# Kernel tuning notes

Hardware: AMD Instinct MI355X
Metric: run time of the kernel (lower is better)

## Reference

```python
import jax, jax.numpy as jnp
import numpy as np

B, A, IN, H, NA = 256, 32, 512, 512, 64


def setup_inputs() -> dict:
    key = jax.random.key(0)
    ks = jax.random.split(key, 9)
    s = 1.0 / np.sqrt(H).astype(np.float32)
    si = 1.0 / np.sqrt(IN).astype(np.float32)
    return {
        "inputs": jax.random.normal(ks[0], (B * A, IN), jnp.float32),
        "hidden_state": jnp.zeros((B, A, H), jnp.float32),
        "W1": jax.random.normal(ks[1], (A, H, IN), jnp.float32) * si,
        "b1": jax.random.normal(ks[2], (A, H), jnp.float32) * si,
        "W_ih": jax.random.normal(ks[3], (A, 3 * H, H), jnp.float32) * s,
        "b_ih": jax.random.normal(ks[4], (A, 3 * H), jnp.float32) * s,
        "W_hh": jax.random.normal(ks[5], (A, 3 * H, H), jnp.float32) * s,
        "b_hh": jax.random.normal(ks[6], (A, 3 * H), jnp.float32) * s,
        "W2": jax.random.normal(ks[7], (A, NA, H), jnp.float32) * s,
        "b2": jax.random.normal(ks[8], (A, NA), jnp.float32) * s,
    }


def reference(inputs, hidden_state, W1, b1, W_ih, b_ih, W_hh, b_hh, W2, b2):
    # inputs: [B*A, IN] -> [B, A, IN]; per-agent distinct weights stacked on axis 0 (a)
    x = inputs.reshape(-1, A, IN)
    h_in = hidden_state  # [B, A, H]
    # fc1 + relu, grouped over agents
    x1 = jax.nn.relu(jnp.einsum('bai,ahi->bah', x, W1) + b1)
    # GRUCell (PyTorch gate layout: r, z, n)
    gx = jnp.einsum('bah,agh->bag', x1, W_ih) + b_ih   # [B, A, 3H]
    gh = jnp.einsum('bah,agh->bag', h_in, W_hh) + b_hh  # [B, A, 3H]
    gx_r, gx_z, gx_n = jnp.split(gx, 3, axis=-1)
    gh_r, gh_z, gh_n = jnp.split(gh, 3, axis=-1)
    r = jax.nn.sigmoid(gx_r + gh_r)
    z = jax.nn.sigmoid(gx_z + gh_z)
    n = jnp.tanh(gx_n + r * gh_n)
    h = (1.0 - z) * n + z * h_in  # [B, A, H]
    # fc2 per agent
    q = jnp.einsum('bah,anh->ban', h, W2) + b2  # [B, A, NA]
    # torch: cat(qs, dim=-1).view(-1, n_actions) == reshape to [B*A, NA]
    return q.reshape(-1, NA), h
```

## Files before the change

kernel.cpp:

```cpp
#include <hip/hip_runtime.h>
#include <hip/hip_bf16.h>


typedef __attribute__((ext_vector_type(8))) __bf16 bf16x8;
typedef __attribute__((ext_vector_type(4))) float  f32x4;

constexpr int NAGENT = 32;
constexpr int KC     = 512;

__device__ __forceinline__ bf16x8 cvt8(const float* p) {
  f32x4 u = *(const f32x4*)p;
  f32x4 v = *(const f32x4*)(p + 4);
  bf16x8 w;
  w[0] = (__bf16)u[0]; w[1] = (__bf16)u[1]; w[2] = (__bf16)u[2]; w[3] = (__bf16)u[3];
  w[4] = (__bf16)v[0]; w[5] = (__bf16)v[1]; w[6] = (__bf16)v[2]; w[7] = (__bf16)v[3];
  return w;
}
__device__ __forceinline__ float sigmoid_f(float x) { return 1.f / (1.f + __expf(-x)); }
__device__ __forceinline__ float tanh_f(float x) {
  float xc = fminf(fmaxf(x, -15.f), 15.f);
  float a = __expf(2.f * xc);
  return (a - 1.f) / (a + 1.f);
}
__device__ __forceinline__ int xcd_swz(int bid, int nwg) {
  return (bid & 7) * (nwg >> 3) + (bid >> 3);
}
__device__ __forceinline__ void lds_barrier() {
  asm volatile("s_waitcnt lgkmcnt(0)" ::: "memory");
  __builtin_amdgcn_s_barrier();
  __builtin_amdgcn_sched_barrier(0);
}


__global__ __launch_bounds__(256) void prep_k(
    const float* __restrict__ hidden, __bf16* __restrict__ AF) {
  const int idx = blockIdx.x * 256 + threadIdx.x;
  const int kc = idx & 63;
  const int row = idx >> 6;
  const int a = row & 31, b = row >> 5;
  bf16x8 v = cvt8(hidden + (size_t)row * KC + kc * 8);
  *(bf16x8*)(AF + ((size_t)(a * 128 + 64 + kc) * 256 + b) * 8) = v;
}

__global__ __launch_bounds__(512, 2) void fc1_k(
    const float* __restrict__ inputs, const float* __restrict__ W1,
    const float* __restrict__ b1, __bf16* __restrict__ AF) {
  const int wg = xcd_swz(blockIdx.x, gridDim.x);
  const int a  = wg >> 3;
  const int n0 = (wg & 7) * 64;

  __shared__ __attribute__((aligned(16))) __bf16 lA[2][256][8][8];
  __shared__ __attribute__((aligned(16))) __bf16 lB[2][64][8][8];

  const int tid = threadIdx.x;
  const int lane = tid & 63;
  const int wave = tid >> 6;
  const int wm = wave >> 1, wn = wave & 1;
  const int lr = lane & 15, lk = lane >> 4;

  int arow[4], aks[4]; size_t aoff[4];
#pragma unroll
  for (int c = 0; c < 4; ++c) {
    const int idx = c * 512 + tid;
    arow[c] = idx >> 3; aks[c] = idx & 7;
    aoff[c] = ((size_t)arow[c] * NAGENT + a) * KC + aks[c] * 8;
  }
  const int brow = tid >> 3, bks = tid & 7;
  const size_t boff = ((size_t)a * 512 + n0 + brow) * KC + bks * 8;

  bf16x8 sA[4], sB;
  auto loadT = [&](int t) {
    const int kb = t * 64;
#pragma unroll
    for (int c = 0; c < 4; ++c) sA[c] = cvt8(inputs + aoff[c] + kb);
    sB = cvt8(W1 + boff + kb);
  };
  auto writeT = [&](int buf) {
#pragma unroll
    for (int c = 0; c < 4; ++c)
      *(bf16x8*)(&lA[buf][arow[c]][aks[c] ^ (arow[c] & 7)][0]) = sA[c];
    *(bf16x8*)(&lB[buf][brow][bks ^ (brow & 7)][0]) = sB;
  };

  f32x4 acc[4][2] = {};
  auto computeT = [&](int buf) {
#pragma unroll
    for (int s = 0; s < 2; ++s) {
      const int ks = s * 4 + lk;
      bf16x8 af[4];
#pragma unroll
      for (int i = 0; i < 4; ++i) {
        const int row = wm * 64 + i * 16 + lr;
        af[i] = *(const bf16x8*)(&lA[buf][row][ks ^ (row & 7)][0]);
      }
#pragma unroll
      for (int cb = 0; cb < 2; ++cb) {
        const int br = wn * 32 + cb * 16 + lr;
        bf16x8 bv = *(const bf16x8*)(&lB[buf][br][ks ^ (br & 7)][0]);
#pragma unroll
        for (int i = 0; i < 4; ++i)
          acc[i][cb] = __builtin_amdgcn_mfma_f32_16x16x32_bf16(af[i], bv, acc[i][cb], 0, 0, 0);
      }
    }
  };

  loadT(0); writeT(0);
  int cur = 0;
#pragma unroll 1
  for (int t = 0; t < 8; ++t) {
    __syncthreads();
    if (t < 7) loadT(t + 1);
    computeT(cur);
    if (t < 7) { writeT(cur ^ 1); cur ^= 1; }
  }

#pragma unroll
  for (int cb = 0; cb < 2; ++cb) {
    const int col = n0 + wn * 32 + cb * 16 + lr;
    const int kc = col >> 3, c7 = col & 7;
    const float bias = b1[(size_t)a * 512 + col];
#pragma unroll
    for (int i = 0; i < 4; ++i) {
      const int r0 = wm * 64 + i * 16 + lk * 4;
#pragma unroll
      for (int e = 0; e < 4; ++e) {
        const float v = fmaxf(acc[i][cb][e] + bias, 0.f);
        AF[((size_t)(a * 128 + kc) * 256 + r0 + e) * 8 + c7] = (__bf16)v;
      }
    }
  }
}

__global__ __launch_bounds__(1024, 4) void gru_k(
    const __bf16* __restrict__ AF,
    const float* __restrict__ Wih, const float* __restrict__ bih,
    const float* __restrict__ Whh, const float* __restrict__ bhh,
    float* __restrict__ hout, __bf16* __restrict__ hbf) {
  const int wg = xcd_swz(blockIdx.x, gridDim.x);
  const int a  = wg >> 3;
  const int n0 = (wg & 7) * 64;

  __shared__ __attribute__((aligned(16))) __bf16 lB[2][192][8][8];

  const int tid = threadIdx.x;
  const int lane = tid & 63;
  const int wave = tid >> 6;
  const int wm = wave >> 1;
  const int wc = wave & 1;
  const int lr = lane & 15, lk = lane >> 4;

  const int br0 = tid >> 3, bks = tid & 7;
  const int br1 = 128 + br0;
  const int boff0 = (a * 1536 + (br0 >> 6) * 512 + n0 + (br0 & 63)) * KC + bks * 8;
  const int boff1 = (a * 1536 + (br1 >> 6) * 512 + n0 + (br1 & 63)) * KC + bks * 8;

  const int aBase = a * 262144 + lk * 2048 + (wm * 32 + lr) * 8;

  bf16x8 sB0, sB1;
  auto loadB = [&](int t) {
    const float* W = (t < 8) ? Wih : Whh;
    const int kb = (t & 7) * 64;
    sB0 = cvt8(W + boff0 + kb);
    if (tid < 512) sB1 = cvt8(W + boff1 + kb);
  };
  auto writeB = [&](int buf) {
    *(bf16x8*)(&lB[buf][br0][bks ^ (br0 & 7)][0]) = sB0;
    if (tid < 512) *(bf16x8*)(&lB[buf][br1][bks ^ (br1 & 7)][0]) = sB1;
  };

  bf16x8 afA[2][2], afB[2][2];
  auto loadA = [&](bf16x8 (&dst)[2][2], int t) {
#pragma unroll
    for (int s = 0; s < 2; ++s)
#pragma unroll
      for (int i = 0; i < 2; ++i)
        dst[s][i] = *(const bf16x8*)(AF + aBase + t * 16384 + s * 8192 + i * 128);
  };

  f32x4 accR[2][2] = {}, accZ[2][2] = {}, accXN[2][2] = {}, accHN[2][2] = {};
  auto compute = [&](int buf, bf16x8 (&af)[2][2], f32x4 (&accN)[2][2]) {
#pragma unroll
    for (int s = 0; s < 2; ++s) {
      const int ks = s * 4 + lk;
#pragma unroll
      for (int cc = 0; cc < 2; ++cc) {
        const int rr = wc * 32 + cc * 16 + lr;
        const int sw = ks ^ (rr & 7);
        bf16x8 bR = *(const bf16x8*)(&lB[buf][rr][sw][0]);
        bf16x8 bZ = *(const bf16x8*)(&lB[buf][64 + rr][sw][0]);
        bf16x8 bN = *(const bf16x8*)(&lB[buf][128 + rr][sw][0]);
#pragma unroll
        for (int i = 0; i < 2; ++i) {
          accR[i][cc] = __builtin_amdgcn_mfma_f32_16x16x32_bf16(af[s][i], bR, accR[i][cc], 0, 0, 0);
          accZ[i][cc] = __builtin_amdgcn_mfma_f32_16x16x32_bf16(af[s][i], bZ, accZ[i][cc], 0, 0, 0);
          accN[i][cc] = __builtin_amdgcn_mfma_f32_16x16x32_bf16(af[s][i], bN, accN[i][cc], 0, 0, 0);
        }
      }
    }
  };

  loadB(0);
  loadA(afA, 0);
  writeB(0);
  lds_barrier();

#pragma unroll
  for (int t = 0; t < 8; ++t) {
    loadB(t + 1);
    if (t & 1) { loadA(afA, t + 1); compute(1, afB, accXN); }
    else       { loadA(afB, t + 1); compute(0, afA, accXN); }
    writeB((t + 1) & 1);
    lds_barrier();
  }
#pragma unroll
  for (int t = 8; t < 16; ++t) {
    if (t < 15) loadB(t + 1);
    if (t & 1) { if (t < 15) loadA(afA, t + 1); compute(1, afB, accHN); }
    else       { loadA(afB, t + 1);             compute(0, afA, accHN); }
    if (t < 15) { writeB((t + 1) & 1); lds_barrier(); }
  }

#pragma unroll
  for (int cc = 0; cc < 2; ++cc) {
    const int col = n0 + wc * 32 + cc * 16 + lr;
    const size_t ab = (size_t)a * 1536 + col;
    const float br_ = bih[ab] + bhh[ab];
    const float bz_ = bih[ab + 512] + bhh[ab + 512];
    const float bxn = bih[ab + 1024];
    const float bhn = bhh[ab + 1024];
    const size_t hfb = ((size_t)(a * 128 + 64 + (col >> 3)) * 256) * 8 + (col & 7);
#pragma unroll
    for (int i = 0; i < 2; ++i) {
      const int r0 = wm * 32 + i * 16 + lk * 4;
#pragma unroll
      for (int e = 0; e < 4; ++e) {
        const float hprev = (float)AF[hfb + (size_t)(r0 + e) * 8];
        const float r = sigmoid_f(accR[i][cc][e] + br_);
        const float z = sigmoid_f(accZ[i][cc][e] + bz_);
        const float n = tanh_f((accXN[i][cc][e] + bxn) + r * (accHN[i][cc][e] + bhn));
        const float h = (1.f - z) * n + z * hprev;
        const size_t o = ((size_t)(r0 + e) * NAGENT + a) * KC + col;
        hout[o] = h;
        hbf[o] = (__bf16)h;
      }
    }
  }
}

template <bool ABF16, int ACT, bool OBF16>
__global__ __launch_bounds__(256) void gemm64(
    const void* __restrict__ Ap, const float* __restrict__ Wp,
    const float* __restrict__ bp, void* __restrict__ Op, const int N) {
  constexpr int BM = 64, MT = 4;
  const int NT = N >> 6;
  const int wg = xcd_swz(blockIdx.x, gridDim.x);
  const int a  = wg / (MT * NT);
  const int rem = wg % (MT * NT);
  const int n0 = (rem / MT) * 64;
  const int b0 = (rem % MT) * BM;

  __shared__ __attribute__((aligned(16))) __bf16 lA[2][4][64][8];
  __shared__ __attribute__((aligned(16))) __bf16 lB[2][4][64][8];

  const int tid = threadIdx.x;
  const int lane = tid & 63;
  const int wn = tid >> 6;
  const int lr = lane & 15, lk = lane >> 4;

  const int ar = tid >> 2, aks = tid & 3;
  const size_t aoff = ((size_t)(b0 + ar) * NAGENT + a) * KC + aks * 8;
  const size_t boff = ((size_t)a * N + n0 + ar) * KC + aks * 8;

  const float*  Af = (const float*)Ap;
  const __bf16* Ab = (const __bf16*)Ap;

  bf16x8 sA, sB;
  auto loadT = [&](int t) {
    if constexpr (ABF16) sA = *(const bf16x8*)(Ab + aoff + t * 32);
    else                 sA = cvt8(Af + aoff + t * 32);
    sB = cvt8(Wp + boff + t * 32);
  };
  auto writeT = [&](int buf) {
    *(bf16x8*)(&lA[buf][aks][ar][0]) = sA;
    *(bf16x8*)(&lB[buf][aks][ar][0]) = sB;
  };

  f32x4 acc[4] = {};
  auto computeT = [&](int buf) {
    bf16x8 bv = *(const bf16x8*)(&lB[buf][lk][wn * 16 + lr][0]);
#pragma unroll
    for (int i = 0; i < 4; ++i) {
      bf16x8 af = *(const bf16x8*)(&lA[buf][lk][i * 16 + lr][0]);
      acc[i] = __builtin_amdgcn_mfma_f32_16x16x32_bf16(af, bv, acc[i], 0, 0, 0);
    }
  };

  loadT(0); writeT(0);
  int cur = 0;
#pragma unroll 1
  for (int t = 0; t < KC / 32; ++t) {
    __syncthreads();
    if (t + 1 < KC / 32) loadT(t + 1);
    computeT(cur);
    if (t + 1 < KC / 32) { writeT(cur ^ 1); cur ^= 1; }
  }

  const int col = n0 + wn * 16 + lr;
  const float bias = bp[(size_t)a * N + col];
#pragma unroll
  for (int i = 0; i < 4; ++i) {
    const int r0 = b0 + i * 16 + lk * 4;
#pragma unroll
    for (int e = 0; e < 4; ++e) {
      float v = acc[i][e] + bias;
      if (ACT == 1) v = fmaxf(v, 0.f);
      const size_t o = ((size_t)(r0 + e) * NAGENT + a) * N + col;
      if constexpr (OBF16) ((__bf16*)Op)[o] = (__bf16)v;
      else                 ((float*)Op)[o]  = v;
    }
  }
}

extern "C" void kernel_launch(void* const* d_in, const int* in_sizes, int n_in,
                              void* d_out, int out_size, void* d_ws, size_t ws_size,
                              hipStream_t stream) {
  const float* inputs = (const float*)d_in[0];
  const float* hidden = (const float*)d_in[1];
  const float* W1   = (const float*)d_in[2];
  const float* b1   = (const float*)d_in[3];
  const float* W_ih = (const float*)d_in[4];
  const float* b_ih = (const float*)d_in[5];
  const float* W_hh = (const float*)d_in[6];
  const float* b_hh = (const float*)d_in[7];
  const float* W2   = (const float*)d_in[8];
  const float* b2   = (const float*)d_in[9];

  float* out_q = (float*)d_out;
  float* out_h = out_q + (size_t)8192 * 64;

  char* ws = (char*)d_ws;
  __bf16* AF  = (__bf16*)(ws);
  __bf16* hbf = (__bf16*)(ws + ((size_t)16 << 20));

  prep_k<<<2048, 256, 0, stream>>>(hidden, AF);
  fc1_k<<<256, 512, 0, stream>>>(inputs, W1, b1, AF);
  gru_k<<<256, 1024, 0, stream>>>(AF, W_ih, b_ih, W_hh, b_hh, out_h, hbf);
  gemm64<true, 0, false><<<128, 256, 0, stream>>>(hbf, W2, b2, out_q, 64);
}
```

Measured before the change: 121.1 us.

## Stream GRU weights to LDS via direct global_load_lds with triple buffering

Replaces the register-staged fp32→bf16 weight load and LDS write in the GRU kernel with direct global-to-LDS DMA of the fp32 weights. Three LDS buffers let the loads run two steps ahead, and the bf16 conversion moves to the fragment read path. This removes VGPR staging and the explicit write phase. In exchange, LDS footprint grows (fp32, three buffers of 192x64), which may hurt occupancy at 1024 threads, and every fragment read now costs extra conversion ALU work and LDS bandwidth. The vmcnt(3) wait also assumes the A-operand loads finish in order.

```diff
diff --git a/kernel.cpp b/kernel.cpp
--- a/kernel.cpp
+++ b/kernel.cpp
@@ -24,11 +24,6 @@
 }
 __device__ __forceinline__ int xcd_swz(int bid, int nwg) {
   return (bid & 7) * (nwg >> 3) + (bid >> 3);
-}
-__device__ __forceinline__ void lds_barrier() {
-  asm volatile("s_waitcnt lgkmcnt(0)" ::: "memory");
-  __builtin_amdgcn_s_barrier();
-  __builtin_amdgcn_sched_barrier(0);
 }
 
 
@@ -140,55 +135,69 @@
   const int a  = wg >> 3;
   const int n0 = (wg & 7) * 64;
 
-  __shared__ __attribute__((aligned(16))) __bf16 lB[2][192][8][8];
+  __shared__ __attribute__((aligned(16))) float lBf[3][192][64];
 
   const int tid = threadIdx.x;
   const int lane = tid & 63;
   const int wave = tid >> 6;
+  const int w4 = wave * 4;
   const int wm = wave >> 1;
   const int wc = wave & 1;
   const int lr = lane & 15, lk = lane >> 4;
 
-  const int br0 = tid >> 3, bks = tid & 7;
-  const int br1 = 128 + br0;
-  const int boff0 = (a * 1536 + (br0 >> 6) * 512 + n0 + (br0 & 63)) * KC + bks * 8;
-  const int boff1 = (a * 1536 + (br1 >> 6) * 512 + n0 + (br1 & 63)) * KC + bks * 8;
+  int boffB[3];
+#pragma unroll
+  for (int c = 0; c < 3; ++c) {
+    const int row = c * 64 + w4 + (lane >> 4);
+    const int s2 = (lane & 15) >> 1, h = lane & 1;
+    const int slot = s2 ^ (row & 7);
+    boffB[c] = (a * 1536 + (row >> 6) * 512 + n0 + (row & 63)) * KC + slot * 8 + h * 4;
+  }
 
   const int aBase = a * 262144 + lk * 2048 + (wm * 32 + lr) * 8;
 
-  bf16x8 sB0, sB1;
-  auto loadB = [&](int t) {
-    const float* W = (t < 8) ? Wih : Whh;
-    const int kb = (t & 7) * 64;
-    sB0 = cvt8(W + boff0 + kb);
-    if (tid < 512) sB1 = cvt8(W + boff1 + kb);
-  };
-  auto writeB = [&](int buf) {
-    *(bf16x8*)(&lB[buf][br0][bks ^ (br0 & 7)][0]) = sB0;
-    if (tid < 512) *(bf16x8*)(&lB[buf][br1][bks ^ (br1 & 7)][0]) = sB1;
-  };
-
-  bf16x8 afA[2][2], afB[2][2];
-  auto loadA = [&](bf16x8 (&dst)[2][2], int t) {
+  auto glB = [&](int tt, int buf) {
+    const float* W = (tt < 8) ? Wih : Whh;
+    const int kb = (tt & 7) * 64;
+#pragma unroll
+    for (int c = 0; c < 3; ++c)
+      __builtin_amdgcn_global_load_lds(
+          (const __attribute__((address_space(1))) unsigned*)(const void*)(W + boffB[c] + kb),
+          (__attribute__((address_space(3))) unsigned*)(void*)&lBf[buf][c * 64 + w4][0],
+          16, 0, 0);
+  };
+
+  auto bfrag = [&](const float* base, int row, int ks) -> bf16x8 {
+    const float* p = base + row * 64 + ((ks ^ (row & 7)) << 3);
+    f32x4 lo = *(const f32x4*)p;
+    f32x4 hi = *(const f32x4*)(p + 4);
+    bf16x8 w;
+    w[0] = (__bf16)lo[0]; w[1] = (__bf16)lo[1]; w[2] = (__bf16)lo[2]; w[3] = (__bf16)lo[3];
+    w[4] = (__bf16)hi[0]; w[5] = (__bf16)hi[1]; w[6] = (__bf16)hi[2]; w[7] = (__bf16)hi[3];
+    return w;
+  };
+
+  f32x4 accR[2][2] = {}, accZ[2][2] = {}, accXN[2][2] = {}, accHN[2][2] = {};
+
+  auto step = [&](int t, f32x4 (&accN)[2][2]) {
+    bf16x8 af[2][2];
 #pragma unroll
     for (int s = 0; s < 2; ++s)
 #pragma unroll
       for (int i = 0; i < 2; ++i)
-        dst[s][i] = *(const bf16x8*)(AF + aBase + t * 16384 + s * 8192 + i * 128);
-  };
-
-  f32x4 accR[2][2] = {}, accZ[2][2] = {}, accXN[2][2] = {}, accHN[2][2] = {};
-  auto compute = [&](int buf, bf16x8 (&af)[2][2], f32x4 (&accN)[2][2]) {
+        af[s][i] = *(const bf16x8*)(AF + aBase + t * 16384 + s * 8192 + i * 128);
+    __builtin_amdgcn_sched_barrier(0);
+    if (t + 2 < 16) glB(t + 2, (t + 2) % 3);
+    const float* base = &lBf[t % 3][0][0];
 #pragma unroll
     for (int s = 0; s < 2; ++s) {
       const int ks = s * 4 + lk;
 #pragma unroll
       for (int cc = 0; cc < 2; ++cc) {
         const int rr = wc * 32 + cc * 16 + lr;
-        const int sw = ks ^ (rr & 7);
-        bf16x8 bR = *(const bf16x8*)(&lB[buf][rr][sw][0]);
-        bf16x8 bZ = *(const bf16x8*)(&lB[buf][64 + rr][sw][0]);
-        bf16x8 bN = *(const bf16x8*)(&lB[buf][128 + rr][sw][0]);
+        bf16x8 bR = bfrag(base, rr, ks);
+        bf16x8 bZ = bfrag(base, 64 + rr, ks);
+        bf16x8 bN = bfrag(base, 128 + rr, ks);
 #pragma unroll
         for (int i = 0; i < 2; ++i) {
           accR[i][cc] = __builtin_amdgcn_mfma_f32_16x16x32_bf16(af[s][i], bR, accR[i][cc], 0, 0, 0);
@@ -197,28 +206,21 @@
         }
       }
     }
-  };
-
-  loadB(0);
-  loadA(afA, 0);
-  writeB(0);
-  lds_barrier();
-
-#pragma unroll
-  for (int t = 0; t < 8; ++t) {
-    loadB(t + 1);
-    if (t & 1) { loadA(afA, t + 1); compute(1, afB, accXN); }
-    else       { loadA(afB, t + 1); compute(0, afA, accXN); }
-    writeB((t + 1) & 1);
-    lds_barrier();
-  }
-#pragma unroll
-  for (int t = 8; t < 16; ++t) {
-    if (t < 15) loadB(t + 1);
-    if (t & 1) { if (t < 15) loadA(afA, t + 1); compute(1, afB, accHN); }
-    else       { loadA(afB, t + 1);             compute(0, afA, accHN); }
-    if (t < 15) { writeB((t + 1) & 1); lds_barrier(); }
-  }
+    asm volatile("s_waitcnt vmcnt(3)" ::: "memory");
+    __builtin_amdgcn_s_barrier();
+    __builtin_amdgcn_sched_barrier(0);
+  };
+
+  glB(0, 0);
+  glB(1, 1);
+  asm volatile("s_waitcnt vmcnt(3)" ::: "memory");
+  __builtin_amdgcn_s_barrier();
+  __builtin_amdgcn_sched_barrier(0);
+
+#pragma unroll
+  for (int t = 0; t < 8; ++t) step(t, accXN);
+#pragma unroll
+  for (int t = 8; t < 16; ++t) step(t, accHN);
 
 #pragma unroll
   for (int cc = 0; cc < 2; ++cc) {
```

Result: faster. 111.9 us (-7.6%).
